# Performance work log

Hardware: AMD Instinct MI355X
Metric: run time of the kernel (lower is better)

## Reference

```python
import jax, jax.numpy as jnp
import numpy as np

N, F_IN, HID, HEADS, E, NG = 50000, 128, 64, 4, 800000, 64
NEG_SLOPE = 0.2


def gat_conv(x, src, dst, W, a_src, a_dst, bias, heads, out_ch, concat):
    n = x.shape[0]
    h = (x @ W).reshape(n, heads, out_ch)                     # [N,H,C]
    # per-node attention logits
    al_src = jnp.sum(h * a_src, axis=-1)                      # [N,H]
    al_dst = jnp.sum(h * a_dst, axis=-1)                      # [N,H]
    e = jax.nn.leaky_relu(al_src[src] + al_dst[dst], NEG_SLOPE)  # [E,H]
    # segment softmax over incoming edges of each destination node
    m = jax.ops.segment_max(e, dst, num_segments=n)           # [N,H]
    m = jnp.where(jnp.isfinite(m), m, 0.0)
    ex = jnp.exp(e - m[dst])
    denom = jax.ops.segment_sum(ex, dst, num_segments=n)      # [N,H]
    alpha = ex / (denom[dst] + 1e-16)                         # [E,H]
    # weighted scatter-sum of gathered source features
    out = jax.ops.segment_sum(h[src] * alpha[:, :, None], dst, num_segments=n)  # [N,H,C]
    if concat:
        out = out.reshape(n, heads * out_ch)
    else:
        out = out.mean(axis=1)
    return out + bias


def setup_inputs() -> dict:
    key = jax.random.key(0)
    ks = jax.random.split(key, 16)
    x = jax.random.normal(ks[0], (N, F_IN), dtype=jnp.float32)
    edge_index = jax.random.randint(ks[1], (2, E), 0, N, dtype=jnp.int32)
    batch = jnp.sort(jax.random.randint(ks[2], (N,), 0, NG, dtype=jnp.int32))
    s1 = 1.0 / np.sqrt(F_IN)
    s2 = 1.0 / np.sqrt(HID * HEADS)
    W1 = jax.random.uniform(ks[3], (F_IN, HEADS * HID), jnp.float32, -s1, s1)
    a_src1 = jax.random.uniform(ks[4], (HEADS, HID), jnp.float32, -s1, s1)
    a_dst1 = jax.random.uniform(ks[5], (HEADS, HID), jnp.float32, -s1, s1)
    b1 = jnp.zeros((HEADS * HID,), jnp.float32)
    W2 = jax.random.uniform(ks[6], (HEADS * HID, HID), jnp.float32, -s2, s2)
    a_src2 = jax.random.uniform(ks[7], (1, HID), jnp.float32, -s2, s2)
    a_dst2 = jax.random.uniform(ks[8], (1, HID), jnp.float32, -s2, s2)
    b2 = jnp.zeros((HID,), jnp.float32)
    s3 = 1.0 / np.sqrt(HID)
    fcW = jax.random.uniform(ks[9], (HID, 1), jnp.float32, -s3, s3)
    fcb = jax.random.uniform(ks[10], (1,), jnp.float32, -s3, s3)
    return {"x": x, "edge_index": edge_index, "batch": batch,
            "W1": W1, "a_src1": a_src1, "a_dst1": a_dst1, "b1": b1,
            "W2": W2, "a_src2": a_src2, "a_dst2": a_dst2, "b2": b2,
            "fcW": fcW, "fcb": fcb}


def reference(x, edge_index, batch, W1, a_src1, a_dst1, b1, W2, a_src2, a_dst2, b2, fcW, fcb):
    n = x.shape[0]
    # PyG GATConv default: add self-loops
    loop = jnp.arange(n, dtype=edge_index.dtype)
    src = jnp.concatenate([edge_index[0], loop])
    dst = jnp.concatenate([edge_index[1], loop])
    # dropout layers are identity at inference
    h = gat_conv(x, src, dst, W1, a_src1, a_dst1, b1, HEADS, HID, True)
    h = jax.nn.elu(h)
    h = gat_conv(h, src, dst, W2, a_src2, a_dst2, b2, 1, HID, False)
    h = jax.nn.elu(h)
    # global mean pool over graphs
    sums = jax.ops.segment_sum(h, batch, num_segments=NG)      # [NG,HID]
    cnts = jax.ops.segment_sum(jnp.ones((n,), h.dtype), batch, num_segments=NG)
    pooled = sums / jnp.maximum(cnts, 1.0)[:, None]
    out = pooled @ fcW + fcb                                    # [NG,1]
    return out.squeeze(-1)
```

## Files before the change

kernel.cpp:

```cpp
#include <hip/hip_runtime.h>
#include <hip/hip_fp16.h>
#include <cstddef>
#include <cstdint>


#define LOG2E 1.4426950408889634f
__device__ __forceinline__ float lrelu02(float x) { return x >= 0.f ? x : 0.2f * x; }
__device__ __forceinline__ float elu1(float x)    { return x > 0.f ? x : expm1f(x); }
__device__ __forceinline__ float fexp(float x)    { return exp2f(x * LOG2E); }

typedef _Float16 f16x8 __attribute__((ext_vector_type(8)));
typedef float    f32x4 __attribute__((ext_vector_type(4)));

__global__ void k_hist(const int* __restrict__ dst, int* __restrict__ cnt,
                       int* __restrict__ rank, int e) {
    int i = blockIdx.x * 256 + threadIdx.x;
    if (i < e) rank[i] = atomicAdd(&cnt[dst[i]], 1);
}

__global__ __launch_bounds__(1024) void k_scan1(const int* __restrict__ cnt,
                                                int* __restrict__ cscan,
                                                int* __restrict__ bsum, int n) {
    __shared__ int ws[16];
    const int t = threadIdx.x, lane = t & 63, wv = t >> 6;
    const int i = blockIdx.x * 1024 + t;
    int v = (i < n) ? cnt[i] : 0;
    int s = v;
#pragma unroll
    for (int d = 1; d < 64; d <<= 1) { int o = __shfl_up(s, d); if (lane >= d) s += o; }
    if (lane == 63) ws[wv] = s;
    __syncthreads();
    if (t < 16) {
        int xx = ws[t];
#pragma unroll
        for (int d = 1; d < 16; d <<= 1) { int o = __shfl_up(xx, d); if (t >= d) xx += o; }
        ws[t] = xx;
        if (t == 15) bsum[blockIdx.x] = xx;
    }
    __syncthreads();
    int incl = s + (wv > 0 ? ws[wv - 1] : 0);
    if (i < n) cscan[i] = incl;
}

__global__ __launch_bounds__(1024) void k_scan2(int* __restrict__ bsum, int nb) {
    __shared__ int ws[16];
    const int t = threadIdx.x, lane = t & 63, wv = t >> 6;
    int v = (t < nb) ? bsum[t] : 0;
    int s = v;
#pragma unroll
    for (int d = 1; d < 64; d <<= 1) { int o = __shfl_up(s, d); if (lane >= d) s += o; }
    if (lane == 63) ws[wv] = s;
    __syncthreads();
    if (t < 16) {
        int xx = ws[t];
#pragma unroll
        for (int d = 1; d < 16; d <<= 1) { int o = __shfl_up(xx, d); if (t >= d) xx += o; }
        ws[t] = xx;
    }
    __syncthreads();
    int incl = s + (wv > 0 ? ws[wv - 1] : 0);
    if (t < nb) bsum[t] = incl - v;
}

__global__ __launch_bounds__(1024) void k_scan3(const int* __restrict__ cscan,
                                                const int* __restrict__ bsum,
                                                int* __restrict__ rowptr, int n) {
    const int i = blockIdx.x * 1024 + threadIdx.x;
    if (i < n) rowptr[i + 1] = cscan[i] + bsum[blockIdx.x];
    if (i == 0) rowptr[0] = 0;
}

__global__ void k_scatter(const int* __restrict__ src, const int* __restrict__ dstArr,
                          const int* __restrict__ rank, const int* __restrict__ rowptr,
                          int* __restrict__ csr, int e) {
    int i = blockIdx.x * 256 + threadIdx.x;
    if (i < e) csr[rowptr[dstArr[i]] + rank[i]] = src[i];
}

__global__ void k_packW(const float* __restrict__ W, __half* __restrict__ Bp, int K, int N) {
    int i = blockIdx.x * 256 + threadIdx.x;
    int total = (K / 32) * (N / 16) * 64;
    if (i >= total) return;
    int c = i & 15, q = (i >> 4) & 3, tnt = i >> 6;
    int nt = tnt % (N / 16), t = tnt / (N / 16);
    int k0 = t * 32 + q * 8, col = nt * 16 + c;
    __half tmp[8];
#pragma unroll
    for (int j = 0; j < 8; ++j) tmp[j] = __float2half(W[(size_t)(k0 + j) * N + col]);
    *reinterpret_cast<int4*>(Bp + (size_t)i * 8) = *reinterpret_cast<int4*>(tmp);
}

template <int K, int N, bool AF32>
__global__ __launch_bounds__(256) void k_gemm_mfma(const void* __restrict__ Av,
                                                   const __half* __restrict__ Bp,
                                                   __half* __restrict__ C, int M) {
    constexpr int NT = N / 16, KT = K / 32;
    const int lane = threadIdx.x & 63;
    const int wv = threadIdx.x >> 6;
    const int row0 = (blockIdx.x * 4 + wv) * 16;
    if (row0 >= M) return;

    f32x4 acc[NT];
#pragma unroll
    for (int nt = 0; nt < NT; ++nt) acc[nt] = (f32x4){0.f, 0.f, 0.f, 0.f};

    const __half* Ah = (const __half*)Av;
    const float*  Af = (const float*)Av;
    const size_t arow = (size_t)(row0 + (lane & 15)) * K + (lane >> 4) * 8;
    const __half* Bb = Bp + (size_t)lane * 8;
#pragma unroll
    for (int t = 0; t < KT; ++t) {
        f16x8 a;
        if constexpr (AF32) {
            float4 u0 = *reinterpret_cast<const float4*>(Af + arow + t * 32);
            float4 u1 = *reinterpret_cast<const float4*>(Af + arow + t * 32 + 4);
            a[0] = (_Float16)u0.x; a[1] = (_Float16)u0.y;
            a[2] = (_Float16)u0.z; a[3] = (_Float16)u0.w;
            a[4] = (_Float16)u1.x; a[5] = (_Float16)u1.y;
            a[6] = (_Float16)u1.z; a[7] = (_Float16)u1.w;
        } else {
            a = *reinterpret_cast<const f16x8*>(Ah + arow + t * 32);
        }
#pragma unroll
        for (int nt = 0; nt < NT; ++nt) {
            f16x8 b = *reinterpret_cast<const f16x8*>(Bb + (size_t)(t * NT + nt) * 512);
            acc[nt] = __builtin_amdgcn_mfma_f32_16x16x32_f16(a, b, acc[nt], 0, 0, 0);
        }
    }
    const int r0 = row0 + (lane >> 4) * 4;
    const int cl = lane & 15;
#pragma unroll
    for (int nt = 0; nt < NT; ++nt) {
        int col = nt * 16 + cl;
#pragma unroll
        for (int j = 0; j < 4; ++j)
            C[(size_t)(r0 + j) * N + col] = __float2half(acc[nt][j]);
    }
}

__device__ __forceinline__ void load_h4(const __half* __restrict__ p, float2& lo, float2& hi) {
    float2 raw = *reinterpret_cast<const float2*>(p);
    __half2* q = reinterpret_cast<__half2*>(&raw);
    lo = __half22float2(q[0]);
    hi = __half22float2(q[1]);
}

__device__ __forceinline__ void h4acc(float2 raw, float w, float& ax, float& ay,
                                      float& az, float& aw2) {
    __half2* q = reinterpret_cast<__half2*>(&raw);
    float2 lo = __half22float2(q[0]), hi = __half22float2(q[1]);
    ax = fmaf(w, lo.x, ax); ay = fmaf(w, lo.y, ay);
    az = fmaf(w, hi.x, az); aw2 = fmaf(w, hi.y, aw2);
}

__global__ void k_al1(const __half* __restrict__ h1, const float* __restrict__ a_src,
                      const float* __restrict__ a_dst, float* __restrict__ als,
                      float* __restrict__ ald, int n) {
    const int lane = threadIdx.x & 63;
    const int node = (blockIdx.x << 2) + (threadIdx.x >> 6);
    if (node >= n) return;
    const int head = lane >> 4;
    float2 lo, hi;
    load_h4(h1 + (size_t)node * 256 + lane * 4, lo, hi);
    float4 av = *reinterpret_cast<const float4*>(a_src + lane * 4);
    float4 dv = *reinterpret_cast<const float4*>(a_dst + lane * 4);
    float ps = lo.x * av.x + lo.y * av.y + hi.x * av.z + hi.y * av.w;
    float pd = lo.x * dv.x + lo.y * dv.y + hi.x * dv.z + hi.y * dv.w;
#pragma unroll
    for (int d = 1; d < 16; d <<= 1) { ps += __shfl_xor(ps, d); pd += __shfl_xor(pd, d); }
    if ((lane & 15) == 0) { als[node * 4 + head] = ps; ald[node * 4 + head] = pd; }
}

__global__ void k_edge1(const __half* __restrict__ h1, const float* __restrict__ als,
                        const float* __restrict__ ald, const int* __restrict__ rowptr,
                        const int* __restrict__ csr, const float* __restrict__ b1,
                        __half* __restrict__ x2, int n) {
    const int lane = threadIdx.x & 63;
    const int node = (blockIdx.x << 2) + (threadIdx.x >> 6);
    if (node >= n) return;
    const int head = lane >> 4;
    const int ch = lane * 4;
    const int e8 = lane & 7, h8 = (lane >> 3) & 3;
    const float adh  = ald[node * 4 + head];
    const float adh8 = ald[node * 4 + h8];
    const int wb = head << 3;
    float axA = 0.f, ayA = 0.f, azA = 0.f, awA = 0.f;
    float axB = 0.f, ayB = 0.f, azB = 0.f, awB = 0.f;
    float wsum = 0.f;
    const int beg = rowptr[node], end = rowptr[node + 1];
    int i = beg;
    for (; i + 8 <= end; i += 8) {
        int s0 = csr[i + 0], s1 = csr[i + 1], s2 = csr[i + 2], s3 = csr[i + 3];
        int s4 = csr[i + 4], s5 = csr[i + 5], s6 = csr[i + 6], s7 = csr[i + 7];
        float2 r0 = *reinterpret_cast<const float2*>(h1 + (size_t)s0 * 256 + ch);
        float2 r1 = *reinterpret_cast<const float2*>(h1 + (size_t)s1 * 256 + ch);
        float2 r2 = *reinterpret_cast<const float2*>(h1 + (size_t)s2 * 256 + ch);
        float2 r3 = *reinterpret_cast<const float2*>(h1 + (size_t)s3 * 256 + ch);
        float2 r4 = *reinterpret_cast<const float2*>(h1 + (size_t)s4 * 256 + ch);
        float2 r5 = *reinterpret_cast<const float2*>(h1 + (size_t)s5 * 256 + ch);
        float2 r6 = *reinterpret_cast<const float2*>(h1 + (size_t)s6 * 256 + ch);
        float2 r7 = *reinterpret_cast<const float2*>(h1 + (size_t)s7 * 256 + ch);
        int se = s0;
        se = (e8 == 1) ? s1 : se; se = (e8 == 2) ? s2 : se; se = (e8 == 3) ? s3 : se;
        se = (e8 == 4) ? s4 : se; se = (e8 == 5) ? s5 : se; se = (e8 == 6) ? s6 : se;
        se = (e8 == 7) ? s7 : se;
        float myw = fexp(lrelu02(als[(size_t)se * 4 + h8] + adh8));
        float w0 = __shfl(myw, wb + 0), w1 = __shfl(myw, wb + 1);
        float w2 = __shfl(myw, wb + 2), w3 = __shfl(myw, wb + 3);
        float w4 = __shfl(myw, wb + 4), w5 = __shfl(myw, wb + 5);
        float w6 = __shfl(myw, wb + 6), w7 = __shfl(myw, wb + 7);
        h4acc(r0, w0, axA, ayA, azA, awA);
        h4acc(r1, w1, axB, ayB, azB, awB);
        h4acc(r2, w2, axA, ayA, azA, awA);
        h4acc(r3, w3, axB, ayB, azB, awB);
        h4acc(r4, w4, axA, ayA, azA, awA);
        h4acc(r5, w5, axB, ayB, azB, awB);
        h4acc(r6, w6, axA, ayA, azA, awA);
        h4acc(r7, w7, axB, ayB, azB, awB);
        wsum += ((w0 + w1) + (w2 + w3)) + ((w4 + w5) + (w6 + w7));
    }
    float ax = axA + axB, ay = ayA + ayB, az = azA + azB, aw = awA + awB;
    for (; i < end; ++i) {
        int s0 = csr[i];
        float w0 = fexp(lrelu02(als[(size_t)s0 * 4 + head] + adh));
        float2 l0, u0;
        load_h4(h1 + (size_t)s0 * 256 + ch, l0, u0);
        ax += w0 * l0.x; ay += w0 * l0.y; az += w0 * u0.x; aw += w0 * u0.y;
        wsum += w0;
    }
    {
        float w0 = fexp(lrelu02(als[node * 4 + head] + adh));
        float2 l0, u0;
        load_h4(h1 + (size_t)node * 256 + ch, l0, u0);
        ax += w0 * l0.x; ay += w0 * l0.y; az += w0 * u0.x; aw += w0 * u0.y;
        wsum += w0;
    }
    const float inv = 1.f / (wsum + 1e-16f);
    float4 bv = *reinterpret_cast<const float4*>(b1 + ch);
    __half2 r0 = __floats2half2_rn(elu1(ax * inv + bv.x), elu1(ay * inv + bv.y));
    __half2 r1 = __floats2half2_rn(elu1(az * inv + bv.z), elu1(aw * inv + bv.w));
    int2 p;
    p.x = *reinterpret_cast<int*>(&r0);
    p.y = *reinterpret_cast<int*>(&r1);
    *reinterpret_cast<int2*>(x2 + (size_t)node * 256 + ch) = p;
}

__global__ void k_al2(const __half* __restrict__ h2, const float* __restrict__ a_src,
                      const float* __restrict__ a_dst, float* __restrict__ als,
                      float* __restrict__ ald, int n) {
    const int lane = threadIdx.x & 63;
    const int node = (blockIdx.x << 2) + (threadIdx.x >> 6);
    if (node >= n) return;
    float hv = __half2float(h2[(size_t)node * 64 + lane]);
    float ps = hv * a_src[lane];
    float pd = hv * a_dst[lane];
#pragma unroll
    for (int d = 1; d < 64; d <<= 1) { ps += __shfl_xor(ps, d); pd += __shfl_xor(pd, d); }
    if (lane == 0) { als[node] = ps; ald[node] = pd; }
}

__global__ void k_edge2(const __half* __restrict__ h2, const float* __restrict__ als,
                        const float* __restrict__ ald, const int* __restrict__ rowptr,
                        const int* __restrict__ csr, const float* __restrict__ b2,
                        float* __restrict__ out2, int n) {
    const int lane = threadIdx.x & 63;
    const int node = (blockIdx.x << 2) + (threadIdx.x >> 6);
    if (node >= n) return;
    const int e8 = lane & 7;
    const float adl = ald[node];
    float accA = 0.f, accB = 0.f, wsum = 0.f;
    const int beg = rowptr[node], end = rowptr[node + 1];
    int i = beg;
    for (; i + 8 <= end; i += 8) {
        int s0 = csr[i + 0], s1 = csr[i + 1], s2 = csr[i + 2], s3 = csr[i + 3];
        int s4 = csr[i + 4], s5 = csr[i + 5], s6 = csr[i + 6], s7 = csr[i + 7];
        float v0 = __half2float(h2[(size_t)s0 * 64 + lane]);
        float v1 = __half2float(h2[(size_t)s1 * 64 + lane]);
        float v2 = __half2float(h2[(size_t)s2 * 64 + lane]);
        float v3 = __half2float(h2[(size_t)s3 * 64 + lane]);
        float v4 = __half2float(h2[(size_t)s4 * 64 + lane]);
        float v5 = __half2float(h2[(size_t)s5 * 64 + lane]);
        float v6 = __half2float(h2[(size_t)s6 * 64 + lane]);
        float v7 = __half2float(h2[(size_t)s7 * 64 + lane]);
        int se = s0;
        se = (e8 == 1) ? s1 : se; se = (e8 == 2) ? s2 : se; se = (e8 == 3) ? s3 : se;
        se = (e8 == 4) ? s4 : se; se = (e8 == 5) ? s5 : se; se = (e8 == 6) ? s6 : se;
        se = (e8 == 7) ? s7 : se;
        float myw = fexp(lrelu02(als[se] + adl));
        float w0 = __shfl(myw, 0), w1 = __shfl(myw, 1), w2 = __shfl(myw, 2), w3 = __shfl(myw, 3);
        float w4 = __shfl(myw, 4), w5 = __shfl(myw, 5), w6 = __shfl(myw, 6), w7 = __shfl(myw, 7);
        accA = fmaf(w0, v0, accA); accB = fmaf(w1, v1, accB);
        accA = fmaf(w2, v2, accA); accB = fmaf(w3, v3, accB);
        accA = fmaf(w4, v4, accA); accB = fmaf(w5, v5, accB);
        accA = fmaf(w6, v6, accA); accB = fmaf(w7, v7, accB);
        wsum += (w0 + w1 + w2 + w3) + (w4 + w5 + w6 + w7);
    }
    float acc = accA + accB;
    for (; i < end; ++i) {
        int s0 = csr[i];
        float w0 = fexp(lrelu02(als[s0] + adl));
        acc += w0 * __half2float(h2[(size_t)s0 * 64 + lane]);
        wsum += w0;
    }
    {
        float w0 = fexp(lrelu02(als[node] + adl));
        acc += w0 * __half2float(h2[(size_t)node * 64 + lane]);
        wsum += w0;
    }
    float o = acc / (wsum + 1e-16f) + b2[lane];
    out2[(size_t)node * 64 + lane] = elu1(o);
}

__global__ __launch_bounds__(1024) void k_pool(const float* __restrict__ out2,
                                               const int* __restrict__ batch,
                                               const float* __restrict__ fcW,
                                               const float* __restrict__ fcb,
                                               float* __restrict__ out, int n) {
    __shared__ float sbuf[16][64];
    const int g = blockIdx.x;
    const int lane = threadIdx.x & 63, wv = threadIdx.x >> 6;
    int lo0 = 0, hi0 = n;
    while (lo0 < hi0) { int mid = (lo0 + hi0) >> 1; if (batch[mid] < g) lo0 = mid + 1; else hi0 = mid; }
    int lo1 = lo0, hi1 = n;
    while (lo1 < hi1) { int mid = (lo1 + hi1) >> 1; if (batch[mid] < g + 1) lo1 = mid + 1; else hi1 = mid; }
    float s0 = 0.f, s1 = 0.f;
    int r = lo0 + wv;
    for (; r + 16 < lo1; r += 32) {
        s0 += out2[(size_t)r * 64 + lane];
        s1 += out2[(size_t)(r + 16) * 64 + lane];
    }
    if (r < lo1) s0 += out2[(size_t)r * 64 + lane];
    sbuf[wv][lane] = s0 + s1;
    __syncthreads();
    if (wv == 0) {
        float s = 0.f;
#pragma unroll
        for (int k = 0; k < 16; ++k) s += sbuf[k][lane];
        float cntf = (float)(lo1 - lo0);
        float pooled = s / fmaxf(cntf, 1.f);
        float v = pooled * fcW[lane];
#pragma unroll
        for (int d = 32; d; d >>= 1) v += __shfl_xor(v, d);
        if (lane == 0) out[g] = v + fcb[0];
    }
}

extern "C" void kernel_launch(void* const* d_in, const int* in_sizes, int n_in,
                              void* d_out, int out_size, void* d_ws, size_t ws_size,
                              hipStream_t stream) {
    const float* x      = (const float*)d_in[0];
    const int*   ei     = (const int*)  d_in[1];
    const int*   batch  = (const int*)  d_in[2];
    const float* W1     = (const float*)d_in[3];
    const float* a_src1 = (const float*)d_in[4];
    const float* a_dst1 = (const float*)d_in[5];
    const float* b1     = (const float*)d_in[6];
    const float* W2     = (const float*)d_in[7];
    const float* a_src2 = (const float*)d_in[8];
    const float* a_dst2 = (const float*)d_in[9];
    const float* b2     = (const float*)d_in[10];
    const float* fcW    = (const float*)d_in[11];
    const float* fcb    = (const float*)d_in[12];
    float* out = (float*)d_out;

    const int N = in_sizes[2];
    const int E = in_sizes[1] / 2;
    (void)n_in; (void)ws_size;

    char* ws = (char*)d_ws;
    size_t off = 0;
    auto alloc = [&](size_t bytes) -> char* {
        char* p = ws + off;
        off += (bytes + 255) & ~(size_t)255;
        return p;
    };
    int*    cnt    = (int*)   alloc((size_t)N * 4);
    int*    cscan  = (int*)   alloc((size_t)N * 4);
    int*    bsum   = (int*)   alloc((size_t)1024 * 4);
    int*    rank   = (int*)   alloc((size_t)E * 4);
    int*    rowptr = (int*)   alloc((size_t)(N + 1) * 4);
    int*    csr    = (int*)   alloc((size_t)E * 4);
    __half* W1p    = (__half*)alloc((size_t)128 * 256 * 2);
    __half* W2p    = (__half*)alloc((size_t)256 * 64 * 2);
    __half* h1h    = (__half*)alloc((size_t)N * 256 * 2);
    __half* x2h    = (__half*)alloc((size_t)N * 256 * 2);
    __half* h2h    = (__half*)alloc((size_t)N * 64 * 2);
    float*  out2   = (float*) alloc((size_t)N * 64 * 4);
    float*  als1   = (float*) alloc((size_t)N * 4 * 4);
    float*  ald1   = (float*) alloc((size_t)N * 4 * 4);
    float*  als2   = (float*) alloc((size_t)N * 4);
    float*  ald2   = (float*) alloc((size_t)N * 4);

    hipMemsetAsync(cnt, 0, (size_t)N * 4, stream);
    const int ge = (E + 255) / 256;
    const int nb = (N + 1023) / 1024;
    k_hist<<<ge, 256, 0, stream>>>(ei + E, cnt, rank, E);
    k_scan1<<<nb, 1024, 0, stream>>>(cnt, cscan, bsum, N);
    k_scan2<<<1, 1024, 0, stream>>>(bsum, nb);
    k_scan3<<<nb, 1024, 0, stream>>>(cscan, bsum, rowptr, N);
    k_scatter<<<ge, 256, 0, stream>>>(ei, ei + E, rank, rowptr, csr, E);

    k_packW<<<(4096 + 255) / 256, 256, 0, stream>>>(W1, W1p, 128, 256);
    k_packW<<<(2048 + 255) / 256, 256, 0, stream>>>(W2, W2p, 256, 64);

    const int gw = (N / 16 + 3) / 4;
    k_gemm_mfma<128, 256, true><<<gw, 256, 0, stream>>>(x, W1p, h1h, N);
    const int gn4 = (N + 3) / 4;
    k_al1<<<gn4, 256, 0, stream>>>(h1h, a_src1, a_dst1, als1, ald1, N);
    k_edge1<<<gn4, 256, 0, stream>>>(h1h, als1, ald1, rowptr, csr, b1, x2h, N);

    k_gemm_mfma<256, 64, false><<<gw, 256, 0, stream>>>(x2h, W2p, h2h, N);
    k_al2<<<gn4, 256, 0, stream>>>(h2h, a_src2, a_dst2, als2, ald2, N);
    k_edge2<<<gn4, 256, 0, stream>>>(h2h, als2, ald2, rowptr, csr, b2, out2, N);

    k_pool<<<out_size, 1024, 0, stream>>>(out2, batch, fcW, fcb, out, N);
}
```

Measured before the change: 234.8 us.

## Fuse attention logits into GEMM epilogue, merge packW launches, unify edge tails

Computes the per-node attention logits (als/ald) in the MFMA GEMM epilogue from fp32 accumulators, removing the separate k_al1/k_al2 kernels and their re-read of h. The two weight-packing launches are merged into one kernel. The edge kernels drop their scalar remainder loops and the separate self-loop step; the self-loop is folded into the 8-wide vectorized loop, with padded slots masked to zero weight. Logits now come from fp32 rather than fp16-rounded h, which shifts numerics slightly, and the masked slots issue redundant loads of the node's own row.

```diff
diff --git a/kernel.cpp b/kernel.cpp
--- a/kernel.cpp
+++ b/kernel.cpp
@@ -77,10 +77,8 @@
     if (i < e) csr[rowptr[dstArr[i]] + rank[i]] = src[i];
 }
 
-__global__ void k_packW(const float* __restrict__ W, __half* __restrict__ Bp, int K, int N) {
-    int i = blockIdx.x * 256 + threadIdx.x;
-    int total = (K / 32) * (N / 16) * 64;
-    if (i >= total) return;
+__device__ __forceinline__ void packOne(const float* __restrict__ W, __half* __restrict__ Bp,
+                                        int K, int N, int i) {
     int c = i & 15, q = (i >> 4) & 3, tnt = i >> 6;
     int nt = tnt % (N / 16), t = tnt / (N / 16);
     int k0 = t * 32 + q * 8, col = nt * 16 + c;
@@ -90,10 +88,21 @@
     *reinterpret_cast<int4*>(Bp + (size_t)i * 8) = *reinterpret_cast<int4*>(tmp);
 }
 
-template <int K, int N, bool AF32>
+__global__ void k_packW(const float* __restrict__ W1, __half* __restrict__ B1,
+                        const float* __restrict__ W2, __half* __restrict__ B2) {
+    int i = blockIdx.x * 256 + threadIdx.x;
+    if (i < 4096) packOne(W1, B1, 128, 256, i);
+    else if (i < 4096 + 2048) packOne(W2, B2, 256, 64, i - 4096);
+}
+
+template <int K, int N, bool AF32, int HEADS_>
 __global__ __launch_bounds__(256) void k_gemm_mfma(const void* __restrict__ Av,
                                                    const __half* __restrict__ Bp,
-                                                   __half* __restrict__ C, int M) {
+                                                   __half* __restrict__ C,
+                                                   const float* __restrict__ a_src,
+                                                   const float* __restrict__ a_dst,
+                                                   float* __restrict__ als,
+                                                   float* __restrict__ ald, int M) {
     constexpr int NT = N / 16, KT = K / 32;
     const int lane = threadIdx.x & 63;
     const int wv = threadIdx.x >> 6;
@@ -136,13 +145,32 @@
         for (int j = 0; j < 4; ++j)
             C[(size_t)(r0 + j) * N + col] = __float2half(acc[nt][j]);
     }
-}
-
-__device__ __forceinline__ void load_h4(const __half* __restrict__ p, float2& lo, float2& hi) {
-    float2 raw = *reinterpret_cast<const float2*>(p);
-    __half2* q = reinterpret_cast<__half2*>(&raw);
-    lo = __half22float2(q[0]);
-    hi = __half22float2(q[1]);
+    float av[NT], dv[NT];
+#pragma unroll
+    for (int nt = 0; nt < NT; ++nt) {
+        av[nt] = a_src[nt * 16 + cl];
+        dv[nt] = a_dst[nt * 16 + cl];
+    }
+    constexpr int NTH = NT / HEADS_;
+#pragma unroll
+    for (int j = 0; j < 4; ++j) {
+#pragma unroll
+        for (int h = 0; h < HEADS_; ++h) {
+            float ps = 0.f, pd = 0.f;
+#pragma unroll
+            for (int t = 0; t < NTH; ++t) {
+                ps = fmaf(acc[h * NTH + t][j], av[h * NTH + t], ps);
+                pd = fmaf(acc[h * NTH + t][j], dv[h * NTH + t], pd);
+            }
+#pragma unroll
+            for (int d = 1; d < 16; d <<= 1) { ps += __shfl_xor(ps, d); pd += __shfl_xor(pd, d); }
+            if (cl == 0) {
+                int r = r0 + j;
+                als[(size_t)r * HEADS_ + h] = ps;
+                ald[(size_t)r * HEADS_ + h] = pd;
+            }
+        }
+    }
 }
 
 __device__ __forceinline__ void h4acc(float2 raw, float w, float& ax, float& ay,
@@ -151,24 +179,6 @@
     float2 lo = __half22float2(q[0]), hi = __half22float2(q[1]);
     ax = fmaf(w, lo.x, ax); ay = fmaf(w, lo.y, ay);
     az = fmaf(w, hi.x, az); aw2 = fmaf(w, hi.y, aw2);
-}
-
-__global__ void k_al1(const __half* __restrict__ h1, const float* __restrict__ a_src,
-                      const float* __restrict__ a_dst, float* __restrict__ als,
-                      float* __restrict__ ald, int n) {
-    const int lane = threadIdx.x & 63;
-    const int node = (blockIdx.x << 2) + (threadIdx.x >> 6);
-    if (node >= n) return;
-    const int head = lane >> 4;
-    float2 lo, hi;
-    load_h4(h1 + (size_t)node * 256 + lane * 4, lo, hi);
-    float4 av = *reinterpret_cast<const float4*>(a_src + lane * 4);
-    float4 dv = *reinterpret_cast<const float4*>(a_dst + lane * 4);
-    float ps = lo.x * av.x + lo.y * av.y + hi.x * av.z + hi.y * av.w;
-    float pd = lo.x * dv.x + lo.y * dv.y + hi.x * dv.z + hi.y * dv.w;
-#pragma unroll
-    for (int d = 1; d < 16; d <<= 1) { ps += __shfl_xor(ps, d); pd += __shfl_xor(pd, d); }
-    if ((lane & 15) == 0) { als[node * 4 + head] = ps; ald[node * 4 + head] = pd; }
 }
 
 __global__ void k_edge1(const __half* __restrict__ h1, const float* __restrict__ als,
@@ -178,20 +188,25 @@
     const int lane = threadIdx.x & 63;
     const int node = (blockIdx.x << 2) + (threadIdx.x >> 6);
     if (node >= n) return;
-    const int head = lane >> 4;
     const int ch = lane * 4;
     const int e8 = lane & 7, h8 = (lane >> 3) & 3;
-    const float adh  = ald[node * 4 + head];
     const float adh8 = ald[node * 4 + h8];
+    const int head = lane >> 4;
     const int wb = head << 3;
     float axA = 0.f, ayA = 0.f, azA = 0.f, awA = 0.f;
     float axB = 0.f, ayB = 0.f, azB = 0.f, awB = 0.f;
     float wsum = 0.f;
-    const int beg = rowptr[node], end = rowptr[node + 1];
-    int i = beg;
-    for (; i + 8 <= end; i += 8) {
-        int s0 = csr[i + 0], s1 = csr[i + 1], s2 = csr[i + 2], s3 = csr[i + 3];
-        int s4 = csr[i + 4], s5 = csr[i + 5], s6 = csr[i + 6], s7 = csr[i + 7];
+    const int beg = rowptr[node];
+    const int deg = rowptr[node + 1] - beg;
+    for (int base = 0; base <= deg; base += 8) {
+        int s0 = (base + 0 < deg) ? csr[beg + base + 0] : node;
+        int s1 = (base + 1 < deg) ? csr[beg + base + 1] : node;
+        int s2 = (base + 2 < deg) ? csr[beg + base + 2] : node;
+        int s3 = (base + 3 < deg) ? csr[beg + base + 3] : node;
+        int s4 = (base + 4 < deg) ? csr[beg + base + 4] : node;
+        int s5 = (base + 5 < deg) ? csr[beg + base + 5] : node;
+        int s6 = (base + 6 < deg) ? csr[beg + base + 6] : node;
+        int s7 = (base + 7 < deg) ? csr[beg + base + 7] : node;
         float2 r0 = *reinterpret_cast<const float2*>(h1 + (size_t)s0 * 256 + ch);
         float2 r1 = *reinterpret_cast<const float2*>(h1 + (size_t)s1 * 256 + ch);
         float2 r2 = *reinterpret_cast<const float2*>(h1 + (size_t)s2 * 256 + ch);
@@ -204,7 +219,8 @@
         se = (e8 == 1) ? s1 : se; se = (e8 == 2) ? s2 : se; se = (e8 == 3) ? s3 : se;
         se = (e8 == 4) ? s4 : se; se = (e8 == 5) ? s5 : se; se = (e8 == 6) ? s6 : se;
         se = (e8 == 7) ? s7 : se;
-        float myw = fexp(lrelu02(als[(size_t)se * 4 + h8] + adh8));
+        float myw = (base + e8 <= deg)
+                        ? fexp(lrelu02(als[(size_t)se * 4 + h8] + adh8)) : 0.f;
         float w0 = __shfl(myw, wb + 0), w1 = __shfl(myw, wb + 1);
         float w2 = __shfl(myw, wb + 2), w3 = __shfl(myw, wb + 3);
         float w4 = __shfl(myw, wb + 4), w5 = __shfl(myw, wb + 5);
@@ -220,43 +236,14 @@
         wsum += ((w0 + w1) + (w2 + w3)) + ((w4 + w5) + (w6 + w7));
     }
     float ax = axA + axB, ay = ayA + ayB, az = azA + azB, aw = awA + awB;
-    for (; i < end; ++i) {
-        int s0 = csr[i];
-        float w0 = fexp(lrelu02(als[(size_t)s0 * 4 + head] + adh));
-        float2 l0, u0;
-        load_h4(h1 + (size_t)s0 * 256 + ch, l0, u0);
-        ax += w0 * l0.x; ay += w0 * l0.y; az += w0 * u0.x; aw += w0 * u0.y;
-        wsum += w0;
-    }
-    {
-        float w0 = fexp(lrelu02(als[node * 4 + head] + adh));
-        float2 l0, u0;
-        load_h4(h1 + (size_t)node * 256 + ch, l0, u0);
-        ax += w0 * l0.x; ay += w0 * l0.y; az += w0 * u0.x; aw += w0 * u0.y;
-        wsum += w0;
-    }
     const float inv = 1.f / (wsum + 1e-16f);
     float4 bv = *reinterpret_cast<const float4*>(b1 + ch);
-    __half2 r0 = __floats2half2_rn(elu1(ax * inv + bv.x), elu1(ay * inv + bv.y));
-    __half2 r1 = __floats2half2_rn(elu1(az * inv + bv.z), elu1(aw * inv + bv.w));
+    __half2 o0 = __floats2half2_rn(elu1(ax * inv + bv.x), elu1(ay * inv + bv.y));
+    __half2 o1 = __floats2half2_rn(elu1(az * inv + bv.z), elu1(aw * inv + bv.w));
     int2 p;
-    p.x = *reinterpret_cast<int*>(&r0);
-    p.y = *reinterpret_cast<int*>(&r1);
+    p.x = *reinterpret_cast<int*>(&o0);
+    p.y = *reinterpret_cast<int*>(&o1);
     *reinterpret_cast<int2*>(x2 + (size_t)node * 256 + ch) = p;
-}
-
-__global__ void k_al2(const __half* __restrict__ h2, const float* __restrict__ a_src,
-                      const float* __restrict__ a_dst, float* __restrict__ als,
-                      float* __restrict__ ald, int n) {
-    const int lane = threadIdx.x & 63;
-    const int node = (blockIdx.x << 2) + (threadIdx.x >> 6);
-    if (node >= n) return;
-    float hv = __half2float(h2[(size_t)node * 64 + lane]);
-    float ps = hv * a_src[lane];
-    float pd = hv * a_dst[lane];
-#pragma unroll
-    for (int d = 1; d < 64; d <<= 1) { ps += __shfl_xor(ps, d); pd += __shfl_xor(pd, d); }
-    if (lane == 0) { als[node] = ps; ald[node] = pd; }
 }
 
 __global__ void k_edge2(const __half* __restrict__ h2, const float* __restrict__ als,
@@ -269,11 +256,17 @@
     const int e8 = lane & 7;
     const float adl = ald[node];
     float accA = 0.f, accB = 0.f, wsum = 0.f;
-    const int beg = rowptr[node], end = rowptr[node + 1];
-    int i = beg;
-    for (; i + 8 <= end; i += 8) {
-        int s0 = csr[i + 0], s1 = csr[i + 1], s2 = csr[i + 2], s3 = csr[i + 3];
-        int s4 = csr[i + 4], s5 = csr[i + 5], s6 = csr[i + 6], s7 = csr[i + 7];
+    const int beg = rowptr[node];
+    const int deg = rowptr[node + 1] - beg;
+    for (int base = 0; base <= deg; base += 8) {
+        int s0 = (base + 0 < deg) ? csr[beg + base + 0] : node;
+        int s1 = (base + 1 < deg) ? csr[beg + base + 1] : node;
+        int s2 = (base + 2 < deg) ? csr[beg + base + 2] : node;
+        int s3 = (base + 3 < deg) ? csr[beg + base + 3] : node;
+        int s4 = (base + 4 < deg) ? csr[beg + base + 4] : node;
+        int s5 = (base + 5 < deg) ? csr[beg + base + 5] : node;
+        int s6 = (base + 6 < deg) ? csr[beg + base + 6] : node;
+        int s7 = (base + 7 < deg) ? csr[beg + base + 7] : node;
         float v0 = __half2float(h2[(size_t)s0 * 64 + lane]);
         float v1 = __half2float(h2[(size_t)s1 * 64 + lane]);
         float v2 = __half2float(h2[(size_t)s2 * 64 + lane]);
@@ -286,7 +279,7 @@
         se = (e8 == 1) ? s1 : se; se = (e8 == 2) ? s2 : se; se = (e8 == 3) ? s3 : se;
         se = (e8 == 4) ? s4 : se; se = (e8 == 5) ? s5 : se; se = (e8 == 6) ? s6 : se;
         se = (e8 == 7) ? s7 : se;
-        float myw = fexp(lrelu02(als[se] + adl));
+        float myw = (base + e8 <= deg) ? fexp(lrelu02(als[se] + adl)) : 0.f;
         float w0 = __shfl(myw, 0), w1 = __shfl(myw, 1), w2 = __shfl(myw, 2), w3 = __shfl(myw, 3);
         float w4 = __shfl(myw, 4), w5 = __shfl(myw, 5), w6 = __shfl(myw, 6), w7 = __shfl(myw, 7);
         accA = fmaf(w0, v0, accA); accB = fmaf(w1, v1, accB);
@@ -296,17 +289,6 @@
         wsum += (w0 + w1 + w2 + w3) + (w4 + w5 + w6 + w7);
     }
     float acc = accA + accB;
-    for (; i < end; ++i) {
-        int s0 = csr[i];
-        float w0 = fexp(lrelu02(als[s0] + adl));
-        acc += w0 * __half2float(h2[(size_t)s0 * 64 + lane]);
-        wsum += w0;
-    }
-    {
-        float w0 = fexp(lrelu02(als[node] + adl));
-        acc += w0 * __half2float(h2[(size_t)node * 64 + lane]);
-        wsum += w0;
-    }
     float o = acc / (wsum + 1e-16f) + b2[lane];
     out2[(size_t)node * 64 + lane] = elu1(o);
 }
@@ -379,7 +361,7 @@
     int*    bsum   = (int*)   alloc((size_t)1024 * 4);
     int*    rank   = (int*)   alloc((size_t)E * 4);
     int*    rowptr = (int*)   alloc((size_t)(N + 1) * 4);
-    int*    csr    = (int*)   alloc((size_t)E * 4);
+    int*    csr    = (int*)   alloc((size_t)(E + 8) * 4);
     __half* W1p    = (__half*)alloc((size_t)128 * 256 * 2);
     __half* W2p    = (__half*)alloc((size_t)256 * 64 * 2);
     __half* h1h    = (__half*)alloc((size_t)N * 256 * 2);
@@ -400,17 +382,16 @@
     k_scan3<<<nb, 1024, 0, stream>>>(cscan, bsum, rowptr, N);
     k_scatter<<<ge, 256, 0, stream>>>(ei, ei + E, rank, rowptr, csr, E);
 
-    k_packW<<<(4096 + 255) / 256, 256, 0, stream>>>(W1, W1p, 128, 256);
-    k_packW<<<(2048 + 255) / 256, 256, 0, stream>>>(W2, W2p, 256, 64);
+    k_packW<<<24, 256, 0, stream>>>(W1, W1p, W2, W2p);
 
     const int gw = (N / 16 + 3) / 4;
-    k_gemm_mfma<128, 256, true><<<gw, 256, 0, stream>>>(x, W1p, h1h, N);
     const int gn4 = (N + 3) / 4;
-    k_al1<<<gn4, 256, 0, stream>>>(h1h, a_src1, a_dst1, als1, ald1, N);
+    k_gemm_mfma<128, 256, true, 4><<<gw, 256, 0, stream>>>(x, W1p, h1h,
+                                                           a_src1, a_dst1, als1, ald1, N);
     k_edge1<<<gn4, 256, 0, stream>>>(h1h, als1, ald1, rowptr, csr, b1, x2h, N);
 
-    k_gemm_mfma<256, 64, false><<<gw, 256, 0, stream>>>(x2h, W2p, h2h, N);
-    k_al2<<<gn4, 256, 0, stream>>>(h2h, a_src2, a_dst2, als2, ald2, N);
+    k_gemm_mfma<256, 64, false, 1><<<gw, 256, 0, stream>>>(x2h, W2p, h2h,
+                                                           a_src2, a_dst2, als2, ald2, N);
     k_edge2<<<gn4, 256, 0, stream>>>(h2h, als2, ald2, rowptr, csr, b2, out2, N);
 
     k_pool<<<out_size, 1024, 0, stream>>>(out2, batch, fcW, fcb, out, N);
```

After: 218.2 us. 1.08x faster.
